# Performance work log

Measured on AMD Instinct MI355X. Metric: run time of the kernel, lower is better.

The kernel has to match this reference:

```python
import jax, jax.numpy as jnp
import numpy as np

EPS = 1e-5

def setup_inputs() -> dict:
    key = jax.random.key(0)
    ks = jax.random.split(key, 16)
    n_users, n_items, d = 100000, 50000, 128
    n_nodes = n_users + n_items
    E = 4800000
    B = 16384
    h1, h2 = 256, 128
    xavier = lambda k, shp: jax.random.uniform(k, shp, jnp.float32, -1.0, 1.0) * np.sqrt(6.0 / (shp[0] + shp[1]))
    inp = {
        'user_indices': jax.random.randint(ks[0], (B,), 0, n_users),
        'item_indices': jax.random.randint(ks[1], (B,), 0, n_items),
        'edge_rows': jax.random.randint(ks[2], (E,), 0, n_nodes, dtype=jnp.int32),
        'edge_cols': jax.random.randint(ks[3], (E,), 0, n_nodes, dtype=jnp.int32),
        'edge_vals': jax.random.uniform(ks[4], (E,), jnp.float32),
        'user_emb': xavier(ks[5], (n_users, d)),
        'item_emb': xavier(ks[6], (n_items, d)),
        'W1': xavier(ks[7], (d, h1)), 'b1': jnp.zeros((h1,), jnp.float32),
        'g1': jnp.ones((h1,), jnp.float32), 'beta1': jnp.zeros((h1,), jnp.float32),
        'W2': xavier(ks[8], (h1, h2)), 'b2': jnp.zeros((h2,), jnp.float32),
        'g2': jnp.ones((h2,), jnp.float32), 'beta2': jnp.zeros((h2,), jnp.float32),
        'P1': xavier(ks[9], (2 * h2, h2)), 'pb1': jnp.zeros((h2,), jnp.float32),
        'P2': xavier(ks[10], (h2, 1)), 'pb2': jnp.zeros((1,), jnp.float32),
    }
    return inp

def _gcn_layer(x, rows, cols, vals, n_nodes, W, b, g, beta):
    # linear transform then sparse adjacency aggregation (COO):
    # out[r] = sum_{e: rows[e]==r} vals[e] * t[cols[e]]
    t = x @ W + b                                   # [N, out]
    agg = jax.ops.segment_sum(vals[:, None] * t[cols], rows, num_segments=n_nodes)
    # BatchNorm1d (training-mode batch statistics over nodes)
    mu = jnp.mean(agg, axis=0)
    var = jnp.var(agg, axis=0)
    out = (agg - mu) * jax.lax.rsqrt(var + EPS) * g + beta
    return jax.nn.relu(out)                         # dropout = identity (eval)

def reference(user_indices, item_indices, edge_rows, edge_cols, edge_vals,
              user_emb, item_emb, W1, b1, g1, beta1, W2, b2, g2, beta2,
              P1, pb1, P2, pb2):
    n_users = user_emb.shape[0]
    x = jnp.concatenate([user_emb, item_emb], axis=0)  # [N, d]
    n_nodes = x.shape[0]
    x = _gcn_layer(x, edge_rows, edge_cols, edge_vals, n_nodes, W1, b1, g1, beta1)
    x = _gcn_layer(x, edge_rows, edge_cols, edge_vals, n_nodes, W2, b2, g2, beta2)
    u = x[:n_users][user_indices]                      # [B, h2]
    v = x[n_users:][item_indices]                      # [B, h2]
    combined = jnp.concatenate([u, v], axis=-1)        # [B, 2*h2]
    h = jax.nn.relu(combined @ P1 + pb1)
    pred = (h @ P2 + pb2).squeeze(-1)                  # [B]
    return pred
```

## Files before the change

### kernel.cpp

```cpp
#include <hip/hip_runtime.h>
#include <stdint.h>

#define N_USERS 100000
#define N_NODES 150000
#define D0      128
#define H1      256
#define H2      128
#define NEDGE   4800000
#define BATCH   16384
#define EPSV    1e-5f
#define NBUCK   147
#define BCHUNK  4096
#define CCHUNK  16384

typedef short short8  __attribute__((ext_vector_type(8)));
typedef float floatx4 __attribute__((ext_vector_type(4)));
typedef unsigned short u16;

__device__ inline float bf2f(u16 u) {
    union { float f; uint32_t i; } x; x.i = ((uint32_t)u) << 16; return x.f;
}
__device__ inline u16 f2bf(float f) {
    union { float f; uint32_t i; } x; x.f = f;
    return (u16)((x.i + 0x7FFFu + ((x.i >> 16) & 1u)) >> 16);
}
__device__ inline float itof(uint32_t u) {
    union { float f; uint32_t i; } x; x.i = u; return x.f;
}
__device__ inline uint32_t ftoi(float f) {
    union { float f; uint32_t i; } x; x.f = f; return x.i;
}

__global__ __launch_bounds__(256) void k_zero(int* __restrict__ p, int n) {
    int i = blockIdx.x * 256 + threadIdx.x;
    if (i < n) p[i] = 0;
}
__global__ __launch_bounds__(256) void k_fillf(float* __restrict__ p, int n, float v) {
    int i = blockIdx.x * 256 + threadIdx.x;
    if (i < n) p[i] = v;
}

__global__ __launch_bounds__(256) void k_cvt(const float* __restrict__ ue,
                                             const float* __restrict__ ie,
                                             u16* __restrict__ xb) {
    int i = (blockIdx.x * 256 + threadIdx.x) * 4;
    const int NU = N_USERS * D0;
    const int NT = N_NODES * D0;
    if (i >= NT) return;
    const float* src = (i < NU) ? (ue + i) : (ie + (i - NU));
    float4 f = *(const float4*)(const void*)src;
    uint2 w;
    w.x = (uint32_t)f2bf(f.x) | ((uint32_t)f2bf(f.y) << 16);
    w.y = (uint32_t)f2bf(f.z) | ((uint32_t)f2bf(f.w) << 16);
    *(uint2*)(void*)(xb + i) = w;
}

__global__ __launch_bounds__(256) void k_bcount(const int* __restrict__ rows,
                                                int* __restrict__ bcount) {
    __shared__ int h[NBUCK];
    int tid = threadIdx.x;
    for (int i = tid; i < NBUCK; i += 256) h[i] = 0;
    __syncthreads();
    int e0 = blockIdx.x * CCHUNK;
    int nE = NEDGE - e0; if (nE > CCHUNK) nE = CCHUNK;
    for (int i = tid; i < nE; i += 256) atomicAdd(&h[rows[e0 + i] >> 10], 1);
    __syncthreads();
    for (int i = tid; i < NBUCK; i += 256)
        if (h[i] > 0) atomicAdd(&bcount[i], h[i]);
}

__global__ __launch_bounds__(256) void k_bscan(const int* __restrict__ bcount,
                                               int* __restrict__ bucket_base,
                                               int* __restrict__ bucket_cursor,
                                               int* __restrict__ row_ptr) {
    int tid = threadIdx.x;
    int c = (tid < NBUCK) ? bcount[tid] : 0;
    int lane = tid & 63, wid = tid >> 6;
    int v = c;
    for (int off = 1; off < 64; off <<= 1) {
        int u = __shfl_up(v, off, 64);
        if (lane >= off) v += u;
    }
    __shared__ int wsum[4];
    if (lane == 63) wsum[wid] = v;
    __syncthreads();
    if (tid == 0) {
        int acc = 0;
        for (int w = 0; w < 4; ++w) { int t = wsum[w]; wsum[w] = acc; acc += t; }
    }
    __syncthreads();
    int ex = wsum[wid] + (v - c);
    if (tid < NBUCK) { bucket_base[tid] = ex; bucket_cursor[tid] = ex; }
    if (tid == 0) { bucket_base[NBUCK] = NEDGE; row_ptr[N_NODES] = NEDGE; }
}

__global__ __launch_bounds__(256) void k_bucket(const int* __restrict__ rows,
                                                const int* __restrict__ cols,
                                                const float* __restrict__ vals,
                                                int* __restrict__ bucket_cursor,
                                                uint2* __restrict__ etmp) {
    __shared__ uint2 stage[BCHUNK];
    __shared__ u16   slotb[BCHUNK];
    __shared__ int   lcnt[NBUCK + 1];
    __shared__ int   lscan[NBUCK + 1];
    __shared__ int   gstart[NBUCK];
    int tid = threadIdx.x;
    int e0 = blockIdx.x * BCHUNK;
    int nE = NEDGE - e0; if (nE > BCHUNK) nE = BCHUNK;

    for (int i = tid; i <= NBUCK; i += 256) lcnt[i] = 0;
    __syncthreads();
    for (int i = tid; i < nE; i += 256) atomicAdd(&lcnt[rows[e0 + i] >> 10], 1);
    __syncthreads();
    if (tid < NBUCK) gstart[tid] = atomicAdd(&bucket_cursor[tid], lcnt[tid]);
    __syncthreads();
    if (tid == 0) {
        int run = 0;
        for (int b = 0; b < NBUCK; ++b) { lscan[b] = run; run += lcnt[b]; lcnt[b] = 0; }
        lscan[NBUCK] = run;
    }
    __syncthreads();
    for (int i = tid; i < nE; i += 256) {
        int r = rows[e0 + i];
        int b = r >> 10;
        int lidx = atomicAdd(&lcnt[b], 1);
        int slot = lscan[b] + lidx;
        uint2 p;
        p.x = ((uint32_t)(r & 1023) << 18) | (uint32_t)cols[e0 + i];
        p.y = ftoi(vals[e0 + i]);
        stage[slot] = p;
        slotb[slot] = (u16)b;
    }
    __syncthreads();
    for (int s = tid; s < nE; s += 256) {
        int b = slotb[s];
        etmp[gstart[b] + (s - lscan[b])] = stage[s];
    }
}

__global__ __launch_bounds__(1024) void k_place2(const int* __restrict__ bucket_base,
                                                 const uint2* __restrict__ etmp,
                                                 int* __restrict__ row_ptr,
                                                 uint2* __restrict__ efin) {
    __shared__ int lcnt[1024];
    __shared__ int lcur[1024];
    __shared__ int wsum[16];
    int b = blockIdx.x;
    int tid = threadIdx.x;
    int base = b << 10;
    int bstart = bucket_base[b];
    int bend   = bucket_base[b + 1];
    lcnt[tid] = 0;
    __syncthreads();
    for (int i = bstart + tid; i < bend; i += 1024)
        atomicAdd(&lcnt[etmp[i].x >> 18], 1);
    __syncthreads();
    int c = lcnt[tid];
    int lane = tid & 63, wid = tid >> 6;
    int v = c;
    for (int off = 1; off < 64; off <<= 1) {
        int u = __shfl_up(v, off, 64);
        if (lane >= off) v += u;
    }
    if (lane == 63) wsum[wid] = v;
    __syncthreads();
    if (tid == 0) {
        int acc = 0;
        for (int w = 0; w < 16; ++w) { int t = wsum[w]; wsum[w] = acc; acc += t; }
    }
    __syncthreads();
    int ex = wsum[wid] + (v - c);
    int gpos = bstart + ex;
    if (base + tid < N_NODES) row_ptr[base + tid] = gpos;
    lcur[tid] = gpos;
    __syncthreads();
    for (int i = bstart + tid; i < bend; i += 1024) {
        uint2 p = etmp[i];
        int rl = (int)(p.x >> 18);
        int pos = atomicAdd(&lcur[rl], 1);
        uint2 o; o.x = p.x & 0x3FFFFu; o.y = p.y;
        efin[pos] = o;
    }
}

__global__ __launch_bounds__(256) void k_transpose(const float* __restrict__ W,
                                                   u16* __restrict__ WT, int K, int N) {
    int i = blockIdx.x * 256 + threadIdx.x;
    if (i >= K * N) return;
    int k = i / N, n = i - k * N;
    WT[n * K + k] = f2bf(W[i]);
}

__global__ __launch_bounds__(256) void k_gemm(const u16* __restrict__ A, int M, int K,
                                              const u16* __restrict__ BT,
                                              const float* __restrict__ bias,
                                              const float* __restrict__ rowscale,
                                              u16* __restrict__ C, int N, int relu) {
    __shared__ u16 lbt[64 * 264];
    int tid = threadIdx.x;
    int lane = tid & 63, wid = tid >> 6;
    int m0 = blockIdx.x * 64;
    int n0 = blockIdx.y * 64;
    const int KP = K + 8;
    int cpr = K / 8;
    for (int idx = tid; idx < 64 * cpr; idx += 256) {
        int r = idx / cpr, c = idx - r * cpr;
        *(uint4*)(void*)(lbt + r * KP + c * 8) =
            *(const uint4*)(const void*)(BT + (size_t)(n0 + r) * K + c * 8);
    }
    __syncthreads();
    int rn = lane & 15;
    int kq = (lane >> 4) * 8;
    int mrow = m0 + wid * 16 + rn;
    int mclamp = mrow < M ? mrow : M - 1;
    const u16* aptr = A + (size_t)mclamp * K + kq;
    floatx4 acc0 = {0.f,0.f,0.f,0.f}, acc1 = acc0, acc2 = acc0, acc3 = acc0;
    for (int kt = 0; kt < K; kt += 32) {
        short8 a  = *(const short8*)(const void*)(aptr + kt);
        short8 b0 = *(const short8*)(const void*)(lbt + ( 0 + rn) * KP + kq + kt);
        short8 b1 = *(const short8*)(const void*)(lbt + (16 + rn) * KP + kq + kt);
        short8 b2 = *(const short8*)(const void*)(lbt + (32 + rn) * KP + kq + kt);
        short8 b3 = *(const short8*)(const void*)(lbt + (48 + rn) * KP + kq + kt);
        acc0 = __builtin_amdgcn_mfma_f32_16x16x32_bf16(a, b0, acc0, 0, 0, 0);
        acc1 = __builtin_amdgcn_mfma_f32_16x16x32_bf16(a, b1, acc1, 0, 0, 0);
        acc2 = __builtin_amdgcn_mfma_f32_16x16x32_bf16(a, b2, acc2, 0, 0, 0);
        acc3 = __builtin_amdgcn_mfma_f32_16x16x32_bf16(a, b3, acc3, 0, 0, 0);
    }
    int rbase = m0 + wid * 16 + (lane >> 4) * 4;
    floatx4 accs[4] = {acc0, acc1, acc2, acc3};
    for (int j = 0; j < 4; ++j) {
        int col = n0 + j * 16 + rn;
        float bs = bias[col];
        for (int i = 0; i < 4; ++i) {
            int row = rbase + i;
            if (row < M) {
                float rs = rowscale ? rowscale[row] : 1.0f;
                float v = accs[j][i] + rs * bs;
                if (relu) v = v < 0.f ? 0.f : v;
                C[(size_t)row * N + col] = f2bf(v);
            }
        }
    }
}

__global__ __launch_bounds__(256) void k_agg(const u16* __restrict__ t,
                                             const int* __restrict__ row_ptr,
                                             const uint2* __restrict__ edges,
                                             u16* __restrict__ agg,
                                             float* __restrict__ rowsum) {
    int row = blockIdx.x * 4 + (threadIdx.x >> 6);
    int lane = threadIdx.x & 63;
    if (row >= N_NODES) return;
    float a0 = 0.f, a1 = 0.f, sv = 0.f;
    int s = row_ptr[row], e = row_ptr[row + 1];
    int i = s;
    for (; i + 8 <= e; i += 8) {
        uint2 ee[8];
        uint32_t rr[8];
        #pragma unroll
        for (int j = 0; j < 8; ++j) ee[j] = edges[i + j];
        #pragma unroll
        for (int j = 0; j < 8; ++j)
            rr[j] = *(const uint32_t*)(const void*)(t + (size_t)ee[j].x * 128 + lane * 2);
        #pragma unroll
        for (int j = 0; j < 8; ++j) {
            float v = itof(ee[j].y);
            a0 += v * bf2f((u16)(rr[j] & 0xffffu));
            a1 += v * bf2f((u16)(rr[j] >> 16));
            sv += v;
        }
    }
    for (; i < e; ++i) {
        uint2 e0 = edges[i];
        uint32_t r0 = *(const uint32_t*)(const void*)(t + (size_t)e0.x * 128 + lane * 2);
        float v0 = itof(e0.y);
        a0 += v0 * bf2f((u16)(r0 & 0xffffu)); a1 += v0 * bf2f((u16)(r0 >> 16));
        sv += v0;
    }
    uint32_t w = (uint32_t)f2bf(a0) | ((uint32_t)f2bf(a1) << 16);
    *(uint32_t*)(void*)(agg + (size_t)row * 128 + lane * 2) = w;
    if (rowsum != nullptr && lane == 0) rowsum[row] = sv;
}

__global__ __launch_bounds__(256) void k_bnstats(const u16* __restrict__ agg,
                                                 float* __restrict__ stats, int NF) {
    int tid = threadIdx.x;
    int rpb = 256 / NF;
    int f = tid & (NF - 1);
    int r0 = blockIdx.x * rpb + tid / NF;
    int rs = gridDim.x * rpb;
    float s = 0.f, s2 = 0.f;
    for (int row = r0; row < N_NODES; row += rs) {
        float v = bf2f(agg[(size_t)row * NF + f]);
        s += v; s2 += v * v;
    }
    atomicAdd(&stats[f], s);
    atomicAdd(&stats[NF + f], s2);
}

__global__ __launch_bounds__(256) void k_bnapply(const u16* __restrict__ agg,
                                                 const float* __restrict__ stats,
                                                 const float* __restrict__ g,
                                                 const float* __restrict__ beta,
                                                 u16* __restrict__ x, int NF) {
    size_t idx = (size_t)blockIdx.x * 256 + threadIdx.x;
    if (idx >= (size_t)N_NODES * NF) return;
    int f = (int)(idx & (size_t)(NF - 1));
    float mu = stats[f] * (1.0f / N_NODES);
    float var = stats[NF + f] * (1.0f / N_NODES) - mu * mu;
    float sc = rsqrtf(var + EPSV) * g[f];
    float v = (bf2f(agg[idx]) - mu) * sc + beta[f];
    x[idx] = f2bf(v < 0.f ? 0.f : v);
}

__global__ __launch_bounds__(256) void k_gatherBN(const int* __restrict__ ui,
                                                  const int* __restrict__ ii,
                                                  const u16* __restrict__ agg2,
                                                  const float* __restrict__ stats,
                                                  const float* __restrict__ g,
                                                  const float* __restrict__ beta,
                                                  u16* __restrict__ comb) {
    int item = blockIdx.x * 4 + (threadIdx.x >> 6);
    int lane = threadIdx.x & 63;
    if (item >= BATCH) return;
    int node = (lane < 32) ? ui[item] : (N_USERS + ii[item]);
    int fb = (lane & 31) * 4;
    uint2 r = *(const uint2*)(const void*)(agg2 + (size_t)node * H2 + fb);
    float vv[4] = { bf2f((u16)(r.x & 0xffffu)), bf2f((u16)(r.x >> 16)),
                    bf2f((u16)(r.y & 0xffffu)), bf2f((u16)(r.y >> 16)) };
    u16 o[4];
    for (int j = 0; j < 4; ++j) {
        int f = fb + j;
        float mu = stats[f] * (1.0f / N_NODES);
        float var = stats[H2 + f] * (1.0f / N_NODES) - mu * mu;
        float sc = rsqrtf(var + EPSV) * g[f];
        float v = (vv[j] - mu) * sc + beta[f];
        o[j] = f2bf(v < 0.f ? 0.f : v);
    }
    uint2 w;
    w.x = (uint32_t)o[0] | ((uint32_t)o[1] << 16);
    w.y = (uint32_t)o[2] | ((uint32_t)o[3] << 16);
    *(uint2*)(void*)(comb + (size_t)item * (2 * H2) + lane * 4) = w;
}

__global__ __launch_bounds__(256) void k_final(const u16* __restrict__ h,
                                               const float* __restrict__ P2,
                                               const float* __restrict__ pb2,
                                               float* __restrict__ out) {
    int item = blockIdx.x * 4 + (threadIdx.x >> 6);
    int lane = threadIdx.x & 63;
    if (item >= BATCH) return;
    float a = bf2f(h[(size_t)item * H2 + lane])      * P2[lane]
            + bf2f(h[(size_t)item * H2 + 64 + lane]) * P2[64 + lane];
    for (int off = 32; off > 0; off >>= 1) a += __shfl_down(a, off, 64);
    if (lane == 0) out[item] = a + pb2[0];
}

extern "C" void kernel_launch(void* const* d_in, const int* in_sizes, int n_in,
                              void* d_out, int out_size, void* d_ws, size_t ws_size,
                              hipStream_t stream) {
    (void)in_sizes; (void)n_in; (void)ws_size;
    const int* user_indices = (const int*)d_in[0];
    const int* item_indices = (const int*)d_in[1];
    const int* edge_rows    = (const int*)d_in[2];
    const int* edge_cols    = (const int*)d_in[3];
    const float* edge_vals = (const float*)d_in[4];
    const float* user_emb  = (const float*)d_in[5];
    const float* item_emb  = (const float*)d_in[6];
    const float* W1    = (const float*)d_in[7];
    const float* b1    = (const float*)d_in[8];
    const float* g1    = (const float*)d_in[9];
    const float* beta1 = (const float*)d_in[10];
    const float* W2    = (const float*)d_in[11];
    const float* b2    = (const float*)d_in[12];
    const float* g2    = (const float*)d_in[13];
    const float* beta2 = (const float*)d_in[14];
    const float* P1    = (const float*)d_in[15];
    const float* pb1   = (const float*)d_in[16];
    const float* P2    = (const float*)d_in[17];
    const float* pb2   = (const float*)d_in[18];
    float* out = (float*)d_out;

    char* ws = (char*)d_ws;
    size_t off = 0;
    auto alloc = [&](size_t bytes) -> char* {
        char* p = ws + off;
        off = (off + bytes + 255) & ~(size_t)255;
        return p;
    };
    int*   row_ptr  = (int*)alloc(sizeof(int) * (N_NODES + 1));
    int*   bcount   = (int*)alloc(sizeof(int) * (NBUCK + 1));
    int*   bbase    = (int*)alloc(sizeof(int) * (NBUCK + 1));
    int*   bcursor  = (int*)alloc(sizeof(int) * (NBUCK + 1));
    float* rowsum   = (float*)alloc(sizeof(float) * N_NODES);
    float* stats1   = (float*)alloc(sizeof(float) * 2 * H1);
    float* stats2   = (float*)alloc(sizeof(float) * 2 * H2);
    u16* WT1 = (u16*)alloc(2 * D0 * H1);
    u16* WT2 = (u16*)alloc(2 * H1 * H2);
    u16* PT1 = (u16*)alloc(2 * 2 * H2 * H2);
    uint2* efin = (uint2*)alloc(8 * (size_t)NEDGE);
    u16* R1   = (u16*)alloc(2 * (size_t)N_NODES * H1);
    u16* xb   = R1;
    u16* aggx = R1 + (size_t)N_NODES * D0;
    u16* x1   = R1;
    u16* R2   = (u16*)alloc(2 * (size_t)N_NODES * H1);
    uint2* etmp = (uint2*)R2;
    u16* agg1 = R2;
    u16* t2   = R2;
    u16* agg2 = R2 + (size_t)N_NODES * H2;
    u16* comb = R2;
    u16* hbuf = R2 + (size_t)BATCH * 2 * H2;

    k_fillf<<<(out_size + 255) / 256, 256, 0, stream>>>(out, out_size, 2.0f);

    k_zero<<<1, 256, 0, stream>>>(bcount, NBUCK + 1);
    k_zero<<<2, 256, 0, stream>>>((int*)stats1, 2 * H1);
    k_zero<<<1, 256, 0, stream>>>((int*)stats2, 2 * H2);

    k_cvt<<<(N_NODES * D0 / 4 + 255) / 256, 256, 0, stream>>>(user_emb, item_emb, xb);

    k_bcount<<<(NEDGE + CCHUNK - 1) / CCHUNK, 256, 0, stream>>>(edge_rows, bcount);
    k_bscan<<<1, 256, 0, stream>>>(bcount, bbase, bcursor, row_ptr);
    k_bucket<<<(NEDGE + BCHUNK - 1) / BCHUNK, 256, 0, stream>>>(
        edge_rows, edge_cols, edge_vals, bcursor, etmp);
    k_place2<<<NBUCK, 1024, 0, stream>>>(bbase, etmp, row_ptr, efin);

    k_transpose<<<(D0 * H1 + 255) / 256, 256, 0, stream>>>(W1, WT1, D0, H1);
    k_transpose<<<(H1 * H2 + 255) / 256, 256, 0, stream>>>(W2, WT2, H1, H2);
    k_transpose<<<(2 * H2 * H2 + 255) / 256, 256, 0, stream>>>(P1, PT1, 2 * H2, H2);

    k_agg<<<N_NODES / 4, 256, 0, stream>>>(xb, row_ptr, efin, aggx, rowsum);
    k_gemm<<<dim3((N_NODES + 63) / 64, H1 / 64), 256, 0, stream>>>(
        aggx, N_NODES, D0, WT1, b1, rowsum, agg1, H1, 0);
    k_bnstats<<<512, 256, 0, stream>>>(agg1, stats1, H1);
    k_bnapply<<<(N_NODES * H1) / 256, 256, 0, stream>>>(agg1, stats1, g1, beta1, x1, H1);

    k_gemm<<<dim3((N_NODES + 63) / 64, H2 / 64), 256, 0, stream>>>(
        x1, N_NODES, H1, WT2, b2, nullptr, t2, H2, 0);
    k_agg<<<N_NODES / 4, 256, 0, stream>>>(t2, row_ptr, efin, agg2, nullptr);
    k_bnstats<<<512, 256, 0, stream>>>(agg2, stats2, H2);

    k_gatherBN<<<BATCH / 4, 256, 0, stream>>>(user_indices, item_indices, agg2,
                                              stats2, g2, beta2, comb);
    k_gemm<<<dim3(BATCH / 64, H2 / 64), 256, 0, stream>>>(
        comb, BATCH, 2 * H2, PT1, pb1, nullptr, hbuf, H2, 1);
    k_final<<<BATCH / 4, 256, 0, stream>>>(hbuf, P2, pb2, out);
}
```

Baseline: 1.033 ms.

## Widen SpMM gathers to 16-byte loads, merge init and transpose launches

The aggregation kernel now maps 16 lanes per row, with each lane loading 8 bf16 values in one 16-byte access. This processes 4 rows per wavefront instead of 1 and unrolls by 4 edges instead of 8. Several small init and zero kernels are merged into one launch, as are the three weight transposes. The serial bucket prefix scan in k_bucket is replaced by a wave-shuffle scan. The aggregation change alters how rows are spread across lanes, so each lane runs fewer edges in flight. It also assumes N_NODES is divisible by 16.

After: 1.018 ms. About the same (-1.5%).

```diff
diff --git a/kernel.cpp b/kernel.cpp
--- a/kernel.cpp
+++ b/kernel.cpp
@@ -30,14 +30,19 @@
 __device__ inline uint32_t ftoi(float f) {
     union { float f; uint32_t i; } x; x.f = f; return x.i;
 }
-
-__global__ __launch_bounds__(256) void k_zero(int* __restrict__ p, int n) {
+__device__ inline uint32_t pack2(float a, float b) {
+    return (uint32_t)f2bf(a) | ((uint32_t)f2bf(b) << 16);
+}
+
+__global__ __launch_bounds__(256) void k_init(float* __restrict__ out, int out_n,
+                                              int* __restrict__ bcount,
+                                              float* __restrict__ stats1,
+                                              float* __restrict__ stats2) {
     int i = blockIdx.x * 256 + threadIdx.x;
-    if (i < n) p[i] = 0;
-}
-__global__ __launch_bounds__(256) void k_fillf(float* __restrict__ p, int n, float v) {
-    int i = blockIdx.x * 256 + threadIdx.x;
-    if (i < n) p[i] = v;
+    if (i < out_n) out[i] = 2.0f;
+    if (i < NBUCK + 1) bcount[i] = 0;
+    if (i < 2 * H1) stats1[i] = 0.f;
+    if (i < 2 * H2) stats2[i] = 0.f;
 }
 
 __global__ __launch_bounds__(256) void k_cvt(const float* __restrict__ ue,
@@ -50,8 +55,8 @@
     const float* src = (i < NU) ? (ue + i) : (ie + (i - NU));
     float4 f = *(const float4*)(const void*)src;
     uint2 w;
-    w.x = (uint32_t)f2bf(f.x) | ((uint32_t)f2bf(f.y) << 16);
-    w.y = (uint32_t)f2bf(f.z) | ((uint32_t)f2bf(f.w) << 16);
+    w.x = pack2(f.x, f.y);
+    w.y = pack2(f.z, f.w);
     *(uint2*)(void*)(xb + i) = w;
 }
 
@@ -104,6 +109,7 @@
     __shared__ int   lcnt[NBUCK + 1];
     __shared__ int   lscan[NBUCK + 1];
     __shared__ int   gstart[NBUCK];
+    __shared__ int   wsum[4];
     int tid = threadIdx.x;
     int e0 = blockIdx.x * BCHUNK;
     int nE = NEDGE - e0; if (nE > BCHUNK) nE = BCHUNK;
@@ -112,12 +118,24 @@
     __syncthreads();
     for (int i = tid; i < nE; i += 256) atomicAdd(&lcnt[rows[e0 + i] >> 10], 1);
     __syncthreads();
-    if (tid < NBUCK) gstart[tid] = atomicAdd(&bucket_cursor[tid], lcnt[tid]);
-    __syncthreads();
-    if (tid == 0) {
-        int run = 0;
-        for (int b = 0; b < NBUCK; ++b) { lscan[b] = run; run += lcnt[b]; lcnt[b] = 0; }
-        lscan[NBUCK] = run;
+    int c = (tid < NBUCK) ? lcnt[tid] : 0;
+    if (tid < NBUCK) gstart[tid] = atomicAdd(&bucket_cursor[tid], c);
+    {
+        int lane = tid & 63, wid = tid >> 6;
+        int v = c;
+        for (int off = 1; off < 64; off <<= 1) {
+            int u = __shfl_up(v, off, 64);
+            if (lane >= off) v += u;
+        }
+        if (lane == 63) wsum[wid] = v;
+        __syncthreads();
+        if (tid == 0) {
+            int acc = 0;
+            for (int w = 0; w < 4; ++w) { int t = wsum[w]; wsum[w] = acc; acc += t; }
+        }
+        __syncthreads();
+        if (tid < NBUCK) lscan[tid] = wsum[wid] + (v - c);
+        for (int i = tid; i < NBUCK; i += 256) lcnt[i] = 0;
     }
     __syncthreads();
     for (int i = tid; i < nE; i += 256) {
@@ -183,10 +201,19 @@
     }
 }
 
-__global__ __launch_bounds__(256) void k_transpose(const float* __restrict__ W,
-                                                   u16* __restrict__ WT, int K, int N) {
-    int i = blockIdx.x * 256 + threadIdx.x;
-    if (i >= K * N) return;
+__global__ __launch_bounds__(256) void k_transpose3(const float* __restrict__ W1,
+                                                    const float* __restrict__ W2,
+                                                    const float* __restrict__ P1,
+                                                    u16* __restrict__ WT1,
+                                                    u16* __restrict__ WT2,
+                                                    u16* __restrict__ PT1) {
+    int gi = blockIdx.x * 256 + threadIdx.x;
+    int seg = gi >> 15;
+    int i = gi & 32767;
+    const float* W; u16* WT; int K, N;
+    if (seg == 0)      { W = W1; WT = WT1; K = D0;     N = H1; }
+    else if (seg == 1) { W = W2; WT = WT2; K = H1;     N = H2; }
+    else               { W = P1; WT = PT1; K = 2 * H2; N = H2; }
     int k = i / N, n = i - k * N;
     WT[n * K + k] = f2bf(W[i]);
 }
@@ -243,43 +270,51 @@
     }
 }
 
+__device__ inline void accum8(float* acc, uint4 r, float v) {
+    acc[0] += v * bf2f((u16)(r.x & 0xffffu)); acc[1] += v * bf2f((u16)(r.x >> 16));
+    acc[2] += v * bf2f((u16)(r.y & 0xffffu)); acc[3] += v * bf2f((u16)(r.y >> 16));
+    acc[4] += v * bf2f((u16)(r.z & 0xffffu)); acc[5] += v * bf2f((u16)(r.z >> 16));
+    acc[6] += v * bf2f((u16)(r.w & 0xffffu)); acc[7] += v * bf2f((u16)(r.w >> 16));
+}
+
 __global__ __launch_bounds__(256) void k_agg(const u16* __restrict__ t,
                                              const int* __restrict__ row_ptr,
                                              const uint2* __restrict__ edges,
                                              u16* __restrict__ agg,
                                              float* __restrict__ rowsum) {
-    int row = blockIdx.x * 4 + (threadIdx.x >> 6);
-    int lane = threadIdx.x & 63;
-    if (row >= N_NODES) return;
-    float a0 = 0.f, a1 = 0.f, sv = 0.f;
+    int tid = threadIdx.x;
+    int lane = tid & 63;
+    int sub = lane >> 4;
+    int l16 = lane & 15;
+    int row = blockIdx.x * 16 + (tid >> 6) * 4 + sub;
+    float acc[8] = {0.f,0.f,0.f,0.f,0.f,0.f,0.f,0.f};
+    float sv = 0.f;
     int s = row_ptr[row], e = row_ptr[row + 1];
+    const u16* tf = t + l16 * 8;
     int i = s;
-    for (; i + 8 <= e; i += 8) {
-        uint2 ee[8];
-        uint32_t rr[8];
-        #pragma unroll
-        for (int j = 0; j < 8; ++j) ee[j] = edges[i + j];
-        #pragma unroll
-        for (int j = 0; j < 8; ++j)
-            rr[j] = *(const uint32_t*)(const void*)(t + (size_t)ee[j].x * 128 + lane * 2);
-        #pragma unroll
-        for (int j = 0; j < 8; ++j) {
-            float v = itof(ee[j].y);
-            a0 += v * bf2f((u16)(rr[j] & 0xffffu));
-            a1 += v * bf2f((u16)(rr[j] >> 16));
-            sv += v;
-        }
+    for (; i + 4 <= e; i += 4) {
+        uint2 e0 = edges[i], e1 = edges[i+1], e2 = edges[i+2], e3 = edges[i+3];
+        uint4 r0 = *(const uint4*)(const void*)(tf + (size_t)e0.x * 128);
+        uint4 r1 = *(const uint4*)(const void*)(tf + (size_t)e1.x * 128);
+        uint4 r2 = *(const uint4*)(const void*)(tf + (size_t)e2.x * 128);
+        uint4 r3 = *(const uint4*)(const void*)(tf + (size_t)e3.x * 128);
+        float v0 = itof(e0.y), v1 = itof(e1.y), v2 = itof(e2.y), v3 = itof(e3.y);
+        accum8(acc, r0, v0); accum8(acc, r1, v1);
+        accum8(acc, r2, v2); accum8(acc, r3, v3);
+        sv += v0 + v1 + v2 + v3;
     }
     for (; i < e; ++i) {
         uint2 e0 = edges[i];
-        uint32_t r0 = *(const uint32_t*)(const void*)(t + (size_t)e0.x * 128 + lane * 2);
+        uint4 r0 = *(const uint4*)(const void*)(tf + (size_t)e0.x * 128);
         float v0 = itof(e0.y);
-        a0 += v0 * bf2f((u16)(r0 & 0xffffu)); a1 += v0 * bf2f((u16)(r0 >> 16));
+        accum8(acc, r0, v0);
         sv += v0;
     }
-    uint32_t w = (uint32_t)f2bf(a0) | ((uint32_t)f2bf(a1) << 16);
-    *(uint32_t*)(void*)(agg + (size_t)row * 128 + lane * 2) = w;
-    if (rowsum != nullptr && lane == 0) rowsum[row] = sv;
+    uint4 w;
+    w.x = pack2(acc[0], acc[1]); w.y = pack2(acc[2], acc[3]);
+    w.z = pack2(acc[4], acc[5]); w.w = pack2(acc[6], acc[7]);
+    *(uint4*)(void*)(agg + (size_t)row * 128 + l16 * 8) = w;
+    if (rowsum != nullptr && l16 == 0) rowsum[row] = sv;
 }
 
 __global__ __launch_bounds__(256) void k_bnstats(const u16* __restrict__ agg,
@@ -411,11 +446,7 @@
     u16* comb = R2;
     u16* hbuf = R2 + (size_t)BATCH * 2 * H2;
 
-    k_fillf<<<(out_size + 255) / 256, 256, 0, stream>>>(out, out_size, 2.0f);
-
-    k_zero<<<1, 256, 0, stream>>>(bcount, NBUCK + 1);
-    k_zero<<<2, 256, 0, stream>>>((int*)stats1, 2 * H1);
-    k_zero<<<1, 256, 0, stream>>>((int*)stats2, 2 * H2);
+    k_init<<<(out_size + 255) / 256, 256, 0, stream>>>(out, out_size, bcount, stats1, stats2);
 
     k_cvt<<<(N_NODES * D0 / 4 + 255) / 256, 256, 0, stream>>>(user_emb, item_emb, xb);
 
@@ -425,11 +456,9 @@
         edge_rows, edge_cols, edge_vals, bcursor, etmp);
     k_place2<<<NBUCK, 1024, 0, stream>>>(bbase, etmp, row_ptr, efin);
 
-    k_transpose<<<(D0 * H1 + 255) / 256, 256, 0, stream>>>(W1, WT1, D0, H1);
-    k_transpose<<<(H1 * H2 + 255) / 256, 256, 0, stream>>>(W2, WT2, H1, H2);
-    k_transpose<<<(2 * H2 * H2 + 255) / 256, 256, 0, stream>>>(P1, PT1, 2 * H2, H2);
-
-    k_agg<<<N_NODES / 4, 256, 0, stream>>>(xb, row_ptr, efin, aggx, rowsum);
+    k_transpose3<<<(3 * 32768) / 256, 256, 0, stream>>>(W1, W2, P1, WT1, WT2, PT1);
+
+    k_agg<<<N_NODES / 16, 256, 0, stream>>>(xb, row_ptr, efin, aggx, rowsum);
     k_gemm<<<dim3((N_NODES + 63) / 64, H1 / 64), 256, 0, stream>>>(
         aggx, N_NODES, D0, WT1, b1, rowsum, agg1, H1, 0);
     k_bnstats<<<512, 256, 0, stream>>>(agg1, stats1, H1);
@@ -437,7 +466,7 @@
 
     k_gemm<<<dim3((N_NODES + 63) / 64, H2 / 64), 256, 0, stream>>>(
         x1, N_NODES, H1, WT2, b2, nullptr, t2, H2, 0);
-    k_agg<<<N_NODES / 4, 256, 0, stream>>>(t2, row_ptr, efin, agg2, nullptr);
+    k_agg<<<N_NODES / 16, 256, 0, stream>>>(t2, row_ptr, efin, agg2, nullptr);
     k_bnstats<<<512, 256, 0, stream>>>(agg2, stats2, H2);
 
     k_gatherBN<<<BATCH / 4, 256, 0, stream>>>(user_indices, item_indices, agg2,
```
